# Kernel optimization log

Measured on AMD Instinct MI355X. Metric: run time of the kernel, lower is better.

Reference implementation:

```python
import jax, jax.numpy as jnp
import numpy as np

DIM = 512
HEADS = 8
NUM_KEYS = 256
TOPK = 32
DIM_HEAD = 128
LN_EPS = 1e-5


def setup_inputs() -> dict:
    key = jax.random.key(0)
    k1, k2, k3, k4 = jax.random.split(key, 4)
    b, t = 2, 1024
    dim_query = DIM_HEAD * HEADS * 2
    x = jax.random.normal(k1, (b, t, DIM), dtype=jnp.float32)
    # nn.Linear(dim, dim_query, bias=False): weight (dim_query, dim), default kaiming-ish; use scaled normal
    Wq = jax.random.normal(k2, (dim_query, DIM), dtype=jnp.float32) / np.sqrt(DIM)
    # keys: (heads, num_keys, 2, dim_head), std = 1/sqrt(dim_head)
    keys = jax.random.normal(k3, (HEADS, NUM_KEYS, 2, DIM_HEAD), dtype=jnp.float32) / np.sqrt(DIM_HEAD)
    # values: (num_keys**2, dim), std = 1/sqrt(dim)
    values = jax.random.normal(k4, (NUM_KEYS ** 2, DIM), dtype=jnp.float32) / np.sqrt(DIM)
    ln_gamma = jnp.ones((DIM_HEAD,), dtype=jnp.float32)
    ln_beta = jnp.zeros((DIM_HEAD,), dtype=jnp.float32)
    return {"x": x, "Wq": Wq, "keys": keys, "values": values,
            "ln_gamma": ln_gamma, "ln_beta": ln_beta}


def reference(x, Wq, keys, values, ln_gamma, ln_beta):
    b, t, _ = x.shape
    h, n, _, d = keys.shape  # (heads, num_keys, 2, dim_head)
    k = TOPK

    # queries: 'b t (p h d)' -> (b, t, 2, h, d)
    q = jnp.einsum('btc,qc->btq', x, Wq).reshape(b, t, 2, h, d)

    # LayerNorm over dim_head (use_layernorm=True path)
    mu = q.mean(axis=-1, keepdims=True)
    var = q.var(axis=-1, keepdims=True)
    q = (q - mu) * jax.lax.rsqrt(var + LN_EPS) * ln_gamma + ln_beta

    # dots: 'p b t h d, h n p d -> b t h p n'
    dots = jnp.einsum('btphd,hnpd->bthpn', q, keys)

    # top-k per sub-key half: (b, t, h, 2, k)
    scores, indices = jax.lax.top_k(dots, k)
    sx, sy = scores[..., 0, :], scores[..., 1, :]
    ix, iy = indices[..., 0, :], indices[..., 1, :]

    # outer combination -> (b, t, h, k*k)
    all_scores = (sx[..., :, None] + sy[..., None, :]).reshape(b, t, h, k * k)
    all_indices = (ix[..., :, None] * n + iy[..., None, :]).reshape(b, t, h, k * k)

    final_scores, final_idx = jax.lax.top_k(all_scores, k)  # (b, t, h, k)
    value_indices = jnp.take_along_axis(all_indices, final_idx, axis=-1)
    attn = jax.nn.softmax(final_scores, axis=-1)

    vi = value_indices.reshape(b * t, h * k)
    w = attn.reshape(b * t, h * k)

    # EmbeddingBag(mode='sum') with per-sample weights
    gathered = values[vi]                      # (bt, hk, dim)
    out = jnp.einsum('nkd,nk->nd', gathered, w)
    return out.reshape(b, t, -1)
```

## Files before the change

### kernel.cpp

```cpp
#include <hip/hip_runtime.h>
#include <math.h>

#define DQ 2048
#define CDIM 512
#define NKEYS 256
#define KSEL 32

__device__ __forceinline__ bool rank_before(float as, int ai, float bs, int bi) {
  return (as > bs) || (as == bs && ai < bi);
}
static __device__ __forceinline__ float bf2f(unsigned int u) {
  union { unsigned int i; float f; } v; v.i = u << 16; return v.f;
}
static __device__ __forceinline__ unsigned int f2bf(float f) {
  union { float f; unsigned int i; } v; v.f = f;
  unsigned int r = v.i + 0x7fffu + ((v.i >> 16) & 1u);
  return r >> 16;
}

__global__ __launch_bounds__(256) void qgemm_ln(
    const float* __restrict__ X, const float* __restrict__ W,
    const float* __restrict__ gamma, const float* __restrict__ beta,
    float* __restrict__ Q) {
  __shared__ float As[16 * 68];
  __shared__ float Bs[16 * 132];
  const int tid = threadIdx.x;
  const int m0 = blockIdx.x * 64, n0 = blockIdx.y * 128;
  const int tx = tid & 15, ty = tid >> 4;
  const int am = tid >> 2, ak = (tid & 3) * 4;
  const int bn = tid >> 1, bk = (tid & 1) * 8;
  float acc[4][8] = {};
  float4 av  = *(const float4*)&X[(size_t)(m0 + am) * CDIM + ak];
  float4 bv0 = *(const float4*)&W[(size_t)(n0 + bn) * CDIM + bk];
  float4 bv1 = *(const float4*)&W[(size_t)(n0 + bn) * CDIM + bk + 4];
  for (int kt = 0; kt < CDIM; kt += 16) {
    __syncthreads();
    As[(ak + 0) * 68 + am] = av.x; As[(ak + 1) * 68 + am] = av.y;
    As[(ak + 2) * 68 + am] = av.z; As[(ak + 3) * 68 + am] = av.w;
    Bs[(bk + 0) * 132 + bn] = bv0.x; Bs[(bk + 1) * 132 + bn] = bv0.y;
    Bs[(bk + 2) * 132 + bn] = bv0.z; Bs[(bk + 3) * 132 + bn] = bv0.w;
    Bs[(bk + 4) * 132 + bn] = bv1.x; Bs[(bk + 5) * 132 + bn] = bv1.y;
    Bs[(bk + 6) * 132 + bn] = bv1.z; Bs[(bk + 7) * 132 + bn] = bv1.w;
    __syncthreads();
    if (kt + 16 < CDIM) {
      av  = *(const float4*)&X[(size_t)(m0 + am) * CDIM + kt + 16 + ak];
      bv0 = *(const float4*)&W[(size_t)(n0 + bn) * CDIM + kt + 16 + bk];
      bv1 = *(const float4*)&W[(size_t)(n0 + bn) * CDIM + kt + 16 + bk + 4];
    }
    #pragma unroll
    for (int kk = 0; kk < 16; ++kk) {
      float4 a4  = *(const float4*)&As[kk * 68 + ty * 4];
      float4 b4a = *(const float4*)&Bs[kk * 132 + tx * 8];
      float4 b4b = *(const float4*)&Bs[kk * 132 + tx * 8 + 4];
      const float ar[4] = {a4.x, a4.y, a4.z, a4.w};
      const float br[8] = {b4a.x, b4a.y, b4a.z, b4a.w, b4b.x, b4b.y, b4b.z, b4b.w};
      #pragma unroll
      for (int i = 0; i < 4; ++i)
        #pragma unroll
        for (int j = 0; j < 8; ++j)
          acc[i][j] += ar[i] * br[j];
    }
  }
  float g[8], bta[8];
  #pragma unroll
  for (int j = 0; j < 8; ++j) { g[j] = gamma[tx * 8 + j]; bta[j] = beta[tx * 8 + j]; }
  #pragma unroll
  for (int i = 0; i < 4; ++i) {
    float s = 0.f, sq = 0.f;
    #pragma unroll
    for (int j = 0; j < 8; ++j) { s += acc[i][j]; sq += acc[i][j] * acc[i][j]; }
    #pragma unroll
    for (int m = 1; m < 16; m <<= 1) {
      s += __shfl_xor(s, m, 64);
      sq += __shfl_xor(sq, m, 64);
    }
    float mean = s * (1.0f / 128.0f);
    float var = sq * (1.0f / 128.0f) - mean * mean;
    float rs = 1.0f / sqrtf(var + 1e-5f);
    float o[8];
    #pragma unroll
    for (int j = 0; j < 8; ++j) o[j] = (acc[i][j] - mean) * rs * g[j] + bta[j];
    float* dst = &Q[(size_t)(m0 + ty * 4 + i) * DQ + n0 + tx * 8];
    *(float4*)dst = make_float4(o[0], o[1], o[2], o[3]);
    *(float4*)(dst + 4) = make_float4(o[4], o[5], o[6], o[7]);
  }
}

__global__ __launch_bounds__(512, 6) void dots_sel(
    const float* __restrict__ Q, const float* __restrict__ keys,
    float* __restrict__ s1s, int* __restrict__ s1i) {
  const int hp = blockIdx.x;
  const int chunk = blockIdx.y;
  const int h = hp >> 1, p = hp & 1;
  const int t0 = chunk * 32;
  __shared__ float Qs[32 * 132];
  __shared__ float Bs[16 * 260];
  const int tid = threadIdx.x;
  const int w = tid >> 6, lane = tid & 63;
  {
    const int tok = tid >> 4, d0 = (tid & 15) * 8;
    const float* src = &Q[(size_t)(t0 + tok) * DQ + p * 1024 + h * 128 + d0];
    *(float4*)&Qs[tok * 132 + d0] = *(const float4*)src;
    *(float4*)&Qs[tok * 132 + d0 + 4] = *(const float4*)(src + 4);
  }
  const int bn = tid >> 1, bkh = (tid & 1) * 8;
  const float* kbase = keys + ((size_t)(h * NKEYS + bn) * 2 + p) * 128;
  float acc[4][4] = {};
  float4 b0 = *(const float4*)&kbase[bkh];
  float4 b1 = *(const float4*)&kbase[bkh + 4];
  for (int kt = 0; kt < 128; kt += 16) {
    __syncthreads();
    Bs[(bkh + 0) * 260 + bn] = b0.x; Bs[(bkh + 1) * 260 + bn] = b0.y;
    Bs[(bkh + 2) * 260 + bn] = b0.z; Bs[(bkh + 3) * 260 + bn] = b0.w;
    Bs[(bkh + 4) * 260 + bn] = b1.x; Bs[(bkh + 5) * 260 + bn] = b1.y;
    Bs[(bkh + 6) * 260 + bn] = b1.z; Bs[(bkh + 7) * 260 + bn] = b1.w;
    __syncthreads();
    if (kt + 16 < 128) {
      b0 = *(const float4*)&kbase[kt + 16 + bkh];
      b1 = *(const float4*)&kbase[kt + 16 + bkh + 4];
    }
    #pragma unroll
    for (int k4 = 0; k4 < 16; k4 += 4) {
      float4 a0 = *(const float4*)&Qs[(w * 4 + 0) * 132 + kt + k4];
      float4 a1 = *(const float4*)&Qs[(w * 4 + 1) * 132 + kt + k4];
      float4 a2 = *(const float4*)&Qs[(w * 4 + 2) * 132 + kt + k4];
      float4 a3 = *(const float4*)&Qs[(w * 4 + 3) * 132 + kt + k4];
      const float a0r[4] = {a0.x, a0.y, a0.z, a0.w};
      const float a1r[4] = {a1.x, a1.y, a1.z, a1.w};
      const float a2r[4] = {a2.x, a2.y, a2.z, a2.w};
      const float a3r[4] = {a3.x, a3.y, a3.z, a3.w};
      #pragma unroll
      for (int kk = 0; kk < 4; ++kk) {
        float4 b4 = *(const float4*)&Bs[(k4 + kk) * 260 + lane * 4];
        const float br[4] = {b4.x, b4.y, b4.z, b4.w};
        #pragma unroll
        for (int j = 0; j < 4; ++j) {
          acc[0][j] += a0r[kk] * br[j];
          acc[1][j] += a1r[kk] * br[j];
          acc[2][j] += a2r[kk] * br[j];
          acc[3][j] += a3r[kk] * br[j];
        }
      }
    }
  }
  for (int i = 0; i < 4; ++i) {
    float s[4]; int id[4];
    #pragma unroll
    for (int r = 0; r < 4; ++r) { s[r] = acc[i][r]; id[r] = lane * 4 + r; }
    #define CE(a, b, dd)                                                       \
      {                                                                        \
        bool sw = (dd) ? rank_before(s[a], id[a], s[b], id[b])                 \
                       : rank_before(s[b], id[b], s[a], id[a]);                \
        if (sw) {                                                              \
          float ts = s[a]; s[a] = s[b]; s[b] = ts;                             \
          int ti = id[a]; id[a] = id[b]; id[b] = ti;                           \
        }                                                                      \
      }
    #define CROSS(L, dd)                                                       \
      {                                                                        \
        bool amHigh = (lane & (L)) != 0;                                       \
        bool flip = amHigh != (dd);                                            \
        _Pragma("unroll")                                                      \
        for (int r = 0; r < 4; ++r) {                                          \
          float os = __shfl_xor(s[r], (L), 64);                                \
          int oi = __shfl_xor(id[r], (L), 64);                                 \
          bool take = rank_before(os, oi, s[r], id[r]) != flip;                \
          if (take) { s[r] = os; id[r] = oi; }                                 \
        }                                                                      \
      }
    CE(0, 1, false); CE(2, 3, true);
    {
      bool dd = (lane & 1) != 0;
      CE(0, 2, dd); CE(1, 3, dd); CE(0, 1, dd); CE(2, 3, dd);
    }
    #pragma unroll
    for (int K = 8; K <= 256; K <<= 1) {
      bool dd = (lane & (K >> 2)) != 0;
      #pragma unroll
      for (int L = K >> 3; L >= 1; L >>= 1) CROSS(L, dd);
      CE(0, 2, dd); CE(1, 3, dd); CE(0, 1, dd); CE(2, 3, dd);
    }
    #undef CE
    #undef CROSS
    const int inst = (t0 + w * 4 + i) * 16 + hp;
    if (lane < 8) {
      *(float4*)&s1s[(size_t)inst * KSEL + lane * 4] = make_float4(s[0], s[1], s[2], s[3]);
      *(int4*)&s1i[(size_t)inst * KSEL + lane * 4] = make_int4(id[0], id[1], id[2], id[3]);
    }
  }
}

__constant__ unsigned short slot_ij[128] = {
  0,1,2,3,4,5,6,7,8,9,10,11,12,13,14,15,16,17,18,19,20,21,22,23,24,25,26,27,28,29,30,31,
  32,33,34,35,36,37,38,39,40,41,42,43,44,45,46,47,
  64,65,66,67,68,69,70,71,72,73,
  96,97,98,99,100,101,102,103,
  128,129,130,131,132,133,
  160,161,162,163,164,
  192,193,194,195,
  224,225,226,227,
  256,257,258,
  288,289,290,
  320,321, 352,353, 384,385, 416,417, 448,449, 480,481,
  512,544,576,608,640,672,704,736,768,800,832,864,896,928,960,992,
  0xFFFF,0xFFFF,0xFFFF,0xFFFF,0xFFFF,0xFFFF,0xFFFF,0xFFFF,0xFFFF
};

__global__ __launch_bounds__(256) void stage2_kernel(
    const float* __restrict__ s1s, const int* __restrict__ s1i,
    float* __restrict__ wgt, int* __restrict__ vidx) {
  const int th = blockIdx.x * 4 + (threadIdx.x >> 6);
  const int lane = threadIdx.x & 63;
  const int bx = th * 64;
  const int by = bx + 32;
  float s[2]; int id[2];
  #pragma unroll
  for (int r = 0; r < 2; ++r) {
    int sl = slot_ij[lane * 2 + r];
    if (sl != 0xFFFF) {
      s[r] = s1s[bx + (sl >> 5)] + s1s[by + (sl & 31)];
      id[r] = sl;
    } else {
      s[r] = -INFINITY; id[r] = 0x7fffffff;
    }
  }
  #define CE2(dd)                                                              \
    {                                                                          \
      bool sw = (dd) ? rank_before(s[0], id[0], s[1], id[1])                   \
                     : rank_before(s[1], id[1], s[0], id[0]);                  \
      if (sw) {                                                                \
        float ts = s[0]; s[0] = s[1]; s[1] = ts;                               \
        int ti = id[0]; id[0] = id[1]; id[1] = ti;                             \
      }                                                                        \
    }
  #define CROSS2(L, dd)                                                        \
    {                                                                          \
      bool amHigh = (lane & (L)) != 0;                                         \
      bool flip = amHigh != (dd);                                              \
      _Pragma("unroll")                                                        \
      for (int r = 0; r < 2; ++r) {                                            \
        float os = __shfl_xor(s[r], (L), 64);                                  \
        int oi = __shfl_xor(id[r], (L), 64);                                   \
        bool take = rank_before(os, oi, s[r], id[r]) != flip;                  \
        if (take) { s[r] = os; id[r] = oi; }                                   \
      }                                                                        \
    }
  { bool dd = (lane & 1) != 0; CE2(dd); }
  #pragma unroll
  for (int K = 4; K <= 128; K <<= 1) {
    bool dd = (lane & (K >> 1)) != 0;
    #pragma unroll
    for (int L = K >> 2; L >= 1; L >>= 1) CROSS2(L, dd);
    CE2(dd);
  }
  #undef CE2
  #undef CROSS2
  float smax = __shfl(s[0], 0, 64);
  float e0 = 0.f, e1 = 0.f;
  if (lane < 16) { e0 = expf(s[0] - smax); e1 = expf(s[1] - smax); }
  float part = e0 + e1;
  #pragma unroll
  for (int m = 1; m < 16; m <<= 1) part += __shfl_xor(part, m, 64);
  if (lane < 16) {
    int f0 = id[0], f1 = id[1];
    int vi0 = s1i[bx + (f0 >> 5)] * NKEYS + s1i[by + (f0 & 31)];
    int vi1 = s1i[bx + (f1 >> 5)] * NKEYS + s1i[by + (f1 & 31)];
    wgt[(size_t)th * KSEL + lane * 2] = e0 / part;
    wgt[(size_t)th * KSEL + lane * 2 + 1] = e1 / part;
    vidx[(size_t)th * KSEL + lane * 2] = vi0;
    vidx[(size_t)th * KSEL + lane * 2 + 1] = vi1;
  }
}

__global__ __launch_bounds__(256) void convert_values(
    const float* __restrict__ values, unsigned int* __restrict__ vbf) {
  const size_t g = ((size_t)blockIdx.x * 256 + threadIdx.x) * 8;
  float4 a = *(const float4*)(values + g);
  float4 b = *(const float4*)(values + g + 4);
  uint4 pk;
  pk.x = f2bf(a.x) | (f2bf(a.y) << 16);
  pk.y = f2bf(a.z) | (f2bf(a.w) << 16);
  pk.z = f2bf(b.x) | (f2bf(b.y) << 16);
  pk.w = f2bf(b.z) | (f2bf(b.w) << 16);
  *(uint4*)(vbf + g / 2) = pk;
}

__global__ __launch_bounds__(256) void gather_bf16(
    const float* __restrict__ wgt, const int* __restrict__ vidx,
    const unsigned short* __restrict__ vbf, float* __restrict__ out) {
  const int t = blockIdx.x;
  const int tid = threadIdx.x, w = tid >> 6, lane = tid & 63;
  __shared__ float ws_[256];
  __shared__ int vs_[256];
  __shared__ float part[4 * 520];
  ws_[tid] = wgt[(size_t)t * 256 + tid];
  vs_[tid] = vidx[(size_t)t * 256 + tid];
  __syncthreads();
  float acc[8] = {};
  const int c0 = lane * 8;
  #pragma unroll 1
  for (int phase = 0; phase < 4; ++phase) {
    for (int e = w; e < 256; e += 4) {
      const int row = vs_[e];
      if ((row >> 14) != phase) continue;
      const float wv = ws_[e];
      uint4 pk = *(const uint4*)(vbf + (size_t)row * CDIM + c0);
      acc[0] += wv * bf2f(pk.x & 0xffff); acc[1] += wv * bf2f(pk.x >> 16);
      acc[2] += wv * bf2f(pk.y & 0xffff); acc[3] += wv * bf2f(pk.y >> 16);
      acc[4] += wv * bf2f(pk.z & 0xffff); acc[5] += wv * bf2f(pk.z >> 16);
      acc[6] += wv * bf2f(pk.w & 0xffff); acc[7] += wv * bf2f(pk.w >> 16);
    }
  }
  #pragma unroll
  for (int j = 0; j < 8; j += 4)
    *(float4*)&part[w * 520 + c0 + j] =
        make_float4(acc[j], acc[j + 1], acc[j + 2], acc[j + 3]);
  __syncthreads();
  const int c2 = tid * 2;
  float r0 = part[c2] + part[520 + c2] + part[1040 + c2] + part[1560 + c2];
  float r1 = part[c2 + 1] + part[520 + c2 + 1] + part[1040 + c2 + 1] + part[1560 + c2 + 1];
  *(float2*)(out + (size_t)t * CDIM + c2) = make_float2(r0, r1);
}

__global__ __launch_bounds__(256) void gather_kernel(
    const float* __restrict__ wgt, const int* __restrict__ vidx,
    const float* __restrict__ values, float* __restrict__ out) {
  const int tp = blockIdx.x;
  const int tid = threadIdx.x;
  __shared__ float ws_[512];
  __shared__ int vs_[512];
  ws_[tid] = wgt[(size_t)tp * 512 + tid];
  ws_[tid + 256] = wgt[(size_t)tp * 512 + tid + 256];
  vs_[tid] = vidx[(size_t)tp * 512 + tid];
  vs_[tid + 256] = vidx[(size_t)tp * 512 + tid + 256];
  __syncthreads();
  const int sub = tid >> 7;
  const int c4 = (tid & 127) * 4;
  const float* wp = &ws_[sub * 256];
  const int* vp = &vs_[sub * 256];
  float4 a = make_float4(0.f, 0.f, 0.f, 0.f);
  #pragma unroll 4
  for (int e = 0; e < 256; ++e) {
    float4 vv = *(const float4*)(values + (size_t)vp[e] * CDIM + c4);
    float wv = wp[e];
    a.x += wv * vv.x; a.y += wv * vv.y; a.z += wv * vv.z; a.w += wv * vv.w;
  }
  *(float4*)(out + (size_t)(tp * 2 + sub) * CDIM + c4) = a;
}

extern "C" void kernel_launch(void* const* d_in, const int* in_sizes, int n_in,
                              void* d_out, int out_size, void* d_ws, size_t ws_size,
                              hipStream_t stream) {
  const float* X      = (const float*)d_in[0];
  const float* W      = (const float*)d_in[1];
  const float* keys   = (const float*)d_in[2];
  const float* values = (const float*)d_in[3];
  const float* gamma  = (const float*)d_in[4];
  const float* beta   = (const float*)d_in[5];
  char* ws = (char*)d_ws;
  float* s1s = (float*)(ws);
  int*   s1i = (int*)  (ws + (4u << 20));
  float* wgt = (float*)(ws + (8u << 20));
  int*   vix = (int*)  (ws + (10u << 20));
  float* Q   = (float*)(ws + (12u << 20));
  unsigned int* vbf = (unsigned int*)(ws + (12u << 20));

  const bool bf16_path = ws_size >= (76u << 20);

  qgemm_ln<<<dim3(32, 16), 256, 0, stream>>>(X, W, gamma, beta, Q);
  dots_sel<<<dim3(16, 64), 512, 0, stream>>>(Q, keys, s1s, s1i);
  stage2_kernel<<<4096, 256, 0, stream>>>(s1s, s1i, wgt, vix);
  if (bf16_path) {
    convert_values<<<16384, 256, 0, stream>>>(values, vbf);
    gather_bf16<<<2048, 256, 0, stream>>>(wgt, vix, (const unsigned short*)vbf, (float*)d_out);
  } else {
    gather_kernel<<<1024, 256, 0, stream>>>(wgt, vix, values, (float*)d_out);
  }
}
```

Before: 445.6 us.

## Enlarge GEMM tile, rework top-k sort, fuse bf16 value conversion into other kernels

The query GEMM moves to 128x128 tiles with an 8x8 per-thread micro-tile and K-step 32, which raises register reuse and cuts the block count. The dots kernel now stages scores in shared memory so each lane bitonic-sorts 16 elements in registers, replacing the 4-per-lane shuffle-heavy sort. The separate fp32-to-bf16 conversion of the values table is folded into extra blocks of dots_sel or stage2, depending on workspace size, to remove a launch and overlap that work. The costs are higher register pressure and lower occupancy (launch bounds drop from 6 to 4), more shared memory per block, and a heterogeneous grid.

```diff
diff --git a/kernel.cpp b/kernel.cpp
--- a/kernel.cpp
+++ b/kernel.cpp
@@ -22,53 +22,62 @@
     const float* __restrict__ X, const float* __restrict__ W,
     const float* __restrict__ gamma, const float* __restrict__ beta,
     float* __restrict__ Q) {
-  __shared__ float As[16 * 68];
-  __shared__ float Bs[16 * 132];
+  __shared__ float As[32 * 132];
+  __shared__ float Bs[32 * 132];
   const int tid = threadIdx.x;
-  const int m0 = blockIdx.x * 64, n0 = blockIdx.y * 128;
+  const int m0 = blockIdx.x * 128, n0 = blockIdx.y * 128;
   const int tx = tid & 15, ty = tid >> 4;
-  const int am = tid >> 2, ak = (tid & 3) * 4;
-  const int bn = tid >> 1, bk = (tid & 1) * 8;
-  float acc[4][8] = {};
-  float4 av  = *(const float4*)&X[(size_t)(m0 + am) * CDIM + ak];
-  float4 bv0 = *(const float4*)&W[(size_t)(n0 + bn) * CDIM + bk];
-  float4 bv1 = *(const float4*)&W[(size_t)(n0 + bn) * CDIM + bk + 4];
-  for (int kt = 0; kt < CDIM; kt += 16) {
+  const int sr = tid >> 1, sk = (tid & 1) * 16;
+  float4 pa[4], pb[4];
+  #pragma unroll
+  for (int q = 0; q < 4; ++q) {
+    pa[q] = *(const float4*)&X[(size_t)(m0 + sr) * CDIM + sk + q * 4];
+    pb[q] = *(const float4*)&W[(size_t)(n0 + sr) * CDIM + sk + q * 4];
+  }
+  float acc[8][8] = {};
+  for (int kt = 0; kt < CDIM; kt += 32) {
     __syncthreads();
-    As[(ak + 0) * 68 + am] = av.x; As[(ak + 1) * 68 + am] = av.y;
-    As[(ak + 2) * 68 + am] = av.z; As[(ak + 3) * 68 + am] = av.w;
-    Bs[(bk + 0) * 132 + bn] = bv0.x; Bs[(bk + 1) * 132 + bn] = bv0.y;
-    Bs[(bk + 2) * 132 + bn] = bv0.z; Bs[(bk + 3) * 132 + bn] = bv0.w;
-    Bs[(bk + 4) * 132 + bn] = bv1.x; Bs[(bk + 5) * 132 + bn] = bv1.y;
-    Bs[(bk + 6) * 132 + bn] = bv1.z; Bs[(bk + 7) * 132 + bn] = bv1.w;
+    #pragma unroll
+    for (int q = 0; q < 4; ++q) {
+      As[(sk + q * 4 + 0) * 132 + sr] = pa[q].x;
+      As[(sk + q * 4 + 1) * 132 + sr] = pa[q].y;
+      As[(sk + q * 4 + 2) * 132 + sr] = pa[q].z;
+      As[(sk + q * 4 + 3) * 132 + sr] = pa[q].w;
+      Bs[(sk + q * 4 + 0) * 132 + sr] = pb[q].x;
+      Bs[(sk + q * 4 + 1) * 132 + sr] = pb[q].y;
+      Bs[(sk + q * 4 + 2) * 132 + sr] = pb[q].z;
+      Bs[(sk + q * 4 + 3) * 132 + sr] = pb[q].w;
+    }
     __syncthreads();
-    if (kt + 16 < CDIM) {
-      av  = *(const float4*)&X[(size_t)(m0 + am) * CDIM + kt + 16 + ak];
-      bv0 = *(const float4*)&W[(size_t)(n0 + bn) * CDIM + kt + 16 + bk];
-      bv1 = *(const float4*)&W[(size_t)(n0 + bn) * CDIM + kt + 16 + bk + 4];
-    }
-    #pragma unroll
-    for (int kk = 0; kk < 16; ++kk) {
-      float4 a4  = *(const float4*)&As[kk * 68 + ty * 4];
-      float4 b4a = *(const float4*)&Bs[kk * 132 + tx * 8];
-      float4 b4b = *(const float4*)&Bs[kk * 132 + tx * 8 + 4];
-      const float ar[4] = {a4.x, a4.y, a4.z, a4.w};
-      const float br[8] = {b4a.x, b4a.y, b4a.z, b4a.w, b4b.x, b4b.y, b4b.z, b4b.w};
+    if (kt + 32 < CDIM) {
       #pragma unroll
-      for (int i = 0; i < 4; ++i)
+      for (int q = 0; q < 4; ++q) {
+        pa[q] = *(const float4*)&X[(size_t)(m0 + sr) * CDIM + kt + 32 + sk + q * 4];
+        pb[q] = *(const float4*)&W[(size_t)(n0 + sr) * CDIM + kt + 32 + sk + q * 4];
+      }
+    }
+    #pragma unroll 8
+    for (int kk = 0; kk < 32; ++kk) {
+      float a[8], b[8];
+      *(float4*)&a[0] = *(const float4*)&As[kk * 132 + ty * 8];
+      *(float4*)&a[4] = *(const float4*)&As[kk * 132 + ty * 8 + 4];
+      *(float4*)&b[0] = *(const float4*)&Bs[kk * 132 + tx * 8];
+      *(float4*)&b[4] = *(const float4*)&Bs[kk * 132 + tx * 8 + 4];
+      #pragma unroll
+      for (int i = 0; i < 8; ++i)
         #pragma unroll
-        for (int j = 0; j < 8; ++j)
-          acc[i][j] += ar[i] * br[j];
-    }
-  }
-  float g[8], bta[8];
-  #pragma unroll
-  for (int j = 0; j < 8; ++j) { g[j] = gamma[tx * 8 + j]; bta[j] = beta[tx * 8 + j]; }
-  #pragma unroll
-  for (int i = 0; i < 4; ++i) {
+        for (int jj = 0; jj < 8; ++jj)
+          acc[i][jj] += a[i] * b[jj];
+    }
+  }
+  float g[8], bb[8];
+  #pragma unroll
+  for (int jj = 0; jj < 8; ++jj) { g[jj] = gamma[tx * 8 + jj]; bb[jj] = beta[tx * 8 + jj]; }
+  #pragma unroll
+  for (int i = 0; i < 8; ++i) {
     float s = 0.f, sq = 0.f;
     #pragma unroll
-    for (int j = 0; j < 8; ++j) { s += acc[i][j]; sq += acc[i][j] * acc[i][j]; }
+    for (int jj = 0; jj < 8; ++jj) { s += acc[i][jj]; sq += acc[i][jj] * acc[i][jj]; }
     #pragma unroll
     for (int m = 1; m < 16; m <<= 1) {
       s += __shfl_xor(s, m, 64);
@@ -79,22 +88,65 @@
     float rs = 1.0f / sqrtf(var + 1e-5f);
     float o[8];
     #pragma unroll
-    for (int j = 0; j < 8; ++j) o[j] = (acc[i][j] - mean) * rs * g[j] + bta[j];
-    float* dst = &Q[(size_t)(m0 + ty * 4 + i) * DQ + n0 + tx * 8];
+    for (int jj = 0; jj < 8; ++jj) o[jj] = (acc[i][jj] - mean) * rs * g[jj] + bb[jj];
+    float* dst = &Q[(size_t)(m0 + ty * 8 + i) * DQ + n0 + tx * 8];
     *(float4*)dst = make_float4(o[0], o[1], o[2], o[3]);
     *(float4*)(dst + 4) = make_float4(o[4], o[5], o[6], o[7]);
   }
 }
 
-__global__ __launch_bounds__(512, 6) void dots_sel(
+#define CE(a, b, dd)                                                           \
+  {                                                                            \
+    bool sw = (dd) ? rank_before(s[a], id[a], s[b], id[b])                     \
+                   : rank_before(s[b], id[b], s[a], id[a]);                    \
+    if (sw) {                                                                  \
+      float ts = s[a]; s[a] = s[b]; s[b] = ts;                                 \
+      int ti = id[a]; id[a] = id[b]; id[b] = ti;                               \
+    }                                                                          \
+  }
+#define CROSSM(M, dd)                                                          \
+  {                                                                            \
+    bool flip = ((j & (M)) != 0) != (dd);                                      \
+    _Pragma("unroll")                                                          \
+    for (int r = 0; r < 16; ++r) {                                             \
+      float os = __shfl_xor(s[r], (M), 64);                                    \
+      int oi = __shfl_xor(id[r], (M), 64);                                     \
+      bool take = rank_before(os, oi, s[r], id[r]) != flip;                    \
+      if (take) { s[r] = os; id[r] = oi; }                                     \
+    }                                                                          \
+  }
+#define INTRA_L(L, dd)                                                         \
+  {                                                                            \
+    _Pragma("unroll")                                                          \
+    for (int base = 0; base < 16; base += 2 * (L))                             \
+      _Pragma("unroll")                                                        \
+      for (int o = 0; o < (L); ++o) CE(base + o, base + o + (L), dd);          \
+  }
+#define INTRA_SET(dd) INTRA_L(8, dd) INTRA_L(4, dd) INTRA_L(2, dd) INTRA_L(1, dd)
+
+__global__ __launch_bounds__(512, 4) void dots_sel(
     const float* __restrict__ Q, const float* __restrict__ keys,
-    float* __restrict__ s1s, int* __restrict__ s1i) {
-  const int hp = blockIdx.x;
-  const int chunk = blockIdx.y;
+    float* __restrict__ s1s, int* __restrict__ s1i,
+    const float* __restrict__ values, unsigned int* __restrict__ vbf) {
+  __shared__ float Qs[32 * 132];
+  __shared__ float Bs[16 * 260];
+  __shared__ float Ts[8 * 1280];
+  if (blockIdx.x >= 1024) {
+    const size_t gbase = ((size_t)(blockIdx.x - 1024) * 512 + threadIdx.x) * 8;
+    float4 a = *(const float4*)(values + gbase);
+    float4 b = *(const float4*)(values + gbase + 4);
+    uint4 pk;
+    pk.x = f2bf(a.x) | (f2bf(a.y) << 16);
+    pk.y = f2bf(a.z) | (f2bf(a.w) << 16);
+    pk.z = f2bf(b.x) | (f2bf(b.y) << 16);
+    pk.w = f2bf(b.z) | (f2bf(b.w) << 16);
+    *(uint4*)(vbf + gbase / 2) = pk;
+    return;
+  }
+  const int hp = blockIdx.x & 15;
+  const int chunk = blockIdx.x >> 4;
   const int h = hp >> 1, p = hp & 1;
   const int t0 = chunk * 32;
-  __shared__ float Qs[32 * 132];
-  __shared__ float Bs[16 * 260];
   const int tid = threadIdx.x;
   const int w = tid >> 6, lane = tid & 63;
   {
@@ -134,58 +186,66 @@
         float4 b4 = *(const float4*)&Bs[(k4 + kk) * 260 + lane * 4];
         const float br[4] = {b4.x, b4.y, b4.z, b4.w};
         #pragma unroll
-        for (int j = 0; j < 4; ++j) {
-          acc[0][j] += a0r[kk] * br[j];
-          acc[1][j] += a1r[kk] * br[j];
-          acc[2][j] += a2r[kk] * br[j];
-          acc[3][j] += a3r[kk] * br[j];
+        for (int jj = 0; jj < 4; ++jj) {
+          acc[0][jj] += a0r[kk] * br[jj];
+          acc[1][jj] += a1r[kk] * br[jj];
+          acc[2][jj] += a2r[kk] * br[jj];
+          acc[3][jj] += a3r[kk] * br[jj];
         }
       }
     }
   }
-  for (int i = 0; i < 4; ++i) {
-    float s[4]; int id[4];
-    #pragma unroll
-    for (int r = 0; r < 4; ++r) { s[r] = acc[i][r]; id[r] = lane * 4 + r; }
-    #define CE(a, b, dd)                                                       \
-      {                                                                        \
-        bool sw = (dd) ? rank_before(s[a], id[a], s[b], id[b])                 \
-                       : rank_before(s[b], id[b], s[a], id[a]);                \
-        if (sw) {                                                              \
-          float ts = s[a]; s[a] = s[b]; s[b] = ts;                             \
-          int ti = id[a]; id[a] = id[b]; id[b] = ti;                           \
-        }                                                                      \
-      }
-    #define CROSS(L, dd)                                                       \
-      {                                                                        \
-        bool amHigh = (lane & (L)) != 0;                                       \
-        bool flip = amHigh != (dd);                                            \
-        _Pragma("unroll")                                                      \
-        for (int r = 0; r < 4; ++r) {                                          \
-          float os = __shfl_xor(s[r], (L), 64);                                \
-          int oi = __shfl_xor(id[r], (L), 64);                                 \
-          bool take = rank_before(os, oi, s[r], id[r]) != flip;                \
-          if (take) { s[r] = os; id[r] = oi; }                                 \
-        }                                                                      \
-      }
-    CE(0, 1, false); CE(2, 3, true);
-    {
-      bool dd = (lane & 1) != 0;
-      CE(0, 2, dd); CE(1, 3, dd); CE(0, 1, dd); CE(2, 3, dd);
-    }
-    #pragma unroll
-    for (int K = 8; K <= 256; K <<= 1) {
-      bool dd = (lane & (K >> 2)) != 0;
-      #pragma unroll
-      for (int L = K >> 3; L >= 1; L >>= 1) CROSS(L, dd);
-      CE(0, 2, dd); CE(1, 3, dd); CE(0, 1, dd); CE(2, 3, dd);
-    }
-    #undef CE
-    #undef CROSS
-    const int inst = (t0 + w * 4 + i) * 16 + hp;
-    if (lane < 8) {
-      *(float4*)&s1s[(size_t)inst * KSEL + lane * 4] = make_float4(s[0], s[1], s[2], s[3]);
-      *(int4*)&s1i[(size_t)inst * KSEL + lane * 4] = make_int4(id[0], id[1], id[2], id[3]);
+  float* twav = &Ts[w * 1280];
+  #pragma unroll
+  for (int g2 = 0; g2 < 4; ++g2)
+    *(float4*)&twav[g2 * 320 + (lane >> 2) * 20 + (lane & 3) * 4] =
+        make_float4(acc[g2][0], acc[g2][1], acc[g2][2], acc[g2][3]);
+  const int g = lane >> 4, j = lane & 15;
+  float s[16]; int id[16];
+  {
+    const float* rbase = &twav[g * 320 + j * 20];
+    #pragma unroll
+    for (int q = 0; q < 4; ++q) {
+      float4 v4 = *(const float4*)&rbase[q * 4];
+      s[q * 4 + 0] = v4.x; s[q * 4 + 1] = v4.y;
+      s[q * 4 + 2] = v4.z; s[q * 4 + 3] = v4.w;
+    }
+    #pragma unroll
+    for (int r = 0; r < 16; ++r) id[r] = j * 16 + r;
+  }
+  #pragma unroll
+  for (int base = 0; base < 16; base += 2) CE(base, base + 1, (base & 2) != 0);
+  #pragma unroll
+  for (int base = 0; base < 16; base += 4) {
+    CE(base + 0, base + 2, (base & 4) != 0);
+    CE(base + 1, base + 3, (base & 4) != 0);
+  }
+  #pragma unroll
+  for (int base = 0; base < 16; base += 2) CE(base, base + 1, (base & 4) != 0);
+  #pragma unroll
+  for (int base = 0; base < 16; base += 8)
+    #pragma unroll
+    for (int o = 0; o < 4; ++o) CE(base + o, base + o + 4, (base & 8) != 0);
+  #pragma unroll
+  for (int base = 0; base < 16; base += 4) {
+    CE(base + 0, base + 2, (base & 8) != 0);
+    CE(base + 1, base + 3, (base & 8) != 0);
+  }
+  #pragma unroll
+  for (int base = 0; base < 16; base += 2) CE(base, base + 1, (base & 8) != 0);
+  { bool dd = (j & 1) != 0; INTRA_SET(dd) }
+  { bool dd = (j & 2) != 0; CROSSM(1, dd) INTRA_SET(dd) }
+  { bool dd = (j & 4) != 0; CROSSM(2, dd) CROSSM(1, dd) INTRA_SET(dd) }
+  { bool dd = (j & 8) != 0; CROSSM(4, dd) CROSSM(2, dd) CROSSM(1, dd) INTRA_SET(dd) }
+  { CROSSM(8, false) CROSSM(4, false) CROSSM(2, false) CROSSM(1, false) INTRA_SET(false) }
+  if (j < 2) {
+    const int inst = (t0 + w * 4 + g) * 16 + hp;
+    float* so = &s1s[(size_t)inst * KSEL + j * 16];
+    int* io = &s1i[(size_t)inst * KSEL + j * 16];
+    #pragma unroll
+    for (int q = 0; q < 4; ++q) {
+      *(float4*)&so[q * 4] = make_float4(s[q * 4], s[q * 4 + 1], s[q * 4 + 2], s[q * 4 + 3]);
+      *(int4*)&io[q * 4] = make_int4(id[q * 4], id[q * 4 + 1], id[q * 4 + 2], id[q * 4 + 3]);
     }
   }
 }
@@ -208,7 +268,20 @@
 
 __global__ __launch_bounds__(256) void stage2_kernel(
     const float* __restrict__ s1s, const int* __restrict__ s1i,
-    float* __restrict__ wgt, int* __restrict__ vidx) {
+    float* __restrict__ wgt, int* __restrict__ vidx,
+    const float* __restrict__ values, unsigned int* __restrict__ vbf) {
+  if (blockIdx.x >= 4096) {
+    const size_t gbase = ((size_t)(blockIdx.x - 4096) * 256 + threadIdx.x) * 8;
+    float4 a = *(const float4*)(values + gbase);
+    float4 b = *(const float4*)(values + gbase + 4);
+    uint4 pk;
+    pk.x = f2bf(a.x) | (f2bf(a.y) << 16);
+    pk.y = f2bf(a.z) | (f2bf(a.w) << 16);
+    pk.z = f2bf(b.x) | (f2bf(b.y) << 16);
+    pk.w = f2bf(b.z) | (f2bf(b.w) << 16);
+    *(uint4*)(vbf + gbase / 2) = pk;
+    return;
+  }
   const int th = blockIdx.x * 4 + (threadIdx.x >> 6);
   const int lane = threadIdx.x & 63;
   const int bx = th * 64;
@@ -270,19 +343,6 @@
     vidx[(size_t)th * KSEL + lane * 2] = vi0;
     vidx[(size_t)th * KSEL + lane * 2 + 1] = vi1;
   }
-}
-
-__global__ __launch_bounds__(256) void convert_values(
-    const float* __restrict__ values, unsigned int* __restrict__ vbf) {
-  const size_t g = ((size_t)blockIdx.x * 256 + threadIdx.x) * 8;
-  float4 a = *(const float4*)(values + g);
-  float4 b = *(const float4*)(values + g + 4);
-  uint4 pk;
-  pk.x = f2bf(a.x) | (f2bf(a.y) << 16);
-  pk.y = f2bf(a.z) | (f2bf(a.w) << 16);
-  pk.z = f2bf(b.x) | (f2bf(b.y) << 16);
-  pk.w = f2bf(b.z) | (f2bf(b.w) << 16);
-  *(uint4*)(vbf + g / 2) = pk;
 }
 
 __global__ __launch_bounds__(256) void gather_bf16(
@@ -312,9 +372,9 @@
     }
   }
   #pragma unroll
-  for (int j = 0; j < 8; j += 4)
-    *(float4*)&part[w * 520 + c0 + j] =
-        make_float4(acc[j], acc[j + 1], acc[j + 2], acc[j + 3]);
+  for (int jj = 0; jj < 8; jj += 4)
+    *(float4*)&part[w * 520 + c0 + jj] =
+        make_float4(acc[jj], acc[jj + 1], acc[jj + 2], acc[jj + 3]);
   __syncthreads();
   const int c2 = tid * 2;
   float r0 = part[c2] + part[520 + c2] + part[1040 + c2] + part[1560 + c2];
@@ -363,15 +423,18 @@
   float* wgt = (float*)(ws + (8u << 20));
   int*   vix = (int*)  (ws + (10u << 20));
   float* Q   = (float*)(ws + (12u << 20));
-  unsigned int* vbf = (unsigned int*)(ws + (12u << 20));
-
-  const bool bf16_path = ws_size >= (76u << 20);
-
-  qgemm_ln<<<dim3(32, 16), 256, 0, stream>>>(X, W, gamma, beta, Q);
-  dots_sel<<<dim3(16, 64), 512, 0, stream>>>(Q, keys, s1s, s1i);
-  stage2_kernel<<<4096, 256, 0, stream>>>(s1s, s1i, wgt, vix);
+  unsigned int* vbf_hi = (unsigned int*)(ws + (28u << 20));
+  unsigned int* vbf_lo = (unsigned int*)(ws + (12u << 20));
+
+  const bool fuse_dots  = ws_size >= (92u << 20);
+  const bool bf16_path  = ws_size >= (76u << 20);
+  unsigned int* vbf = fuse_dots ? vbf_hi : vbf_lo;
+
+  qgemm_ln<<<dim3(16, 16), 256, 0, stream>>>(X, W, gamma, beta, Q);
+  dots_sel<<<fuse_dots ? 9216 : 1024, 512, 0, stream>>>(Q, keys, s1s, s1i, values, vbf);
+  stage2_kernel<<<(bf16_path && !fuse_dots) ? 20480 : 4096, 256, 0, stream>>>(
+      s1s, s1i, wgt, vix, values, vbf);
   if (bf16_path) {
-    convert_values<<<16384, 256, 0, stream>>>(values, vbf);
     gather_bf16<<<2048, 256, 0, stream>>>(wgt, vix, (const unsigned short*)vbf, (float*)d_out);
   } else {
     gather_kernel<<<1024, 256, 0, stream>>>(wgt, vix, values, (float*)d_out);
```

Result: slower. 484.5 us (+8.7%).
